# Performance work log

Hardware: AMD Instinct MI355X
Metric: run time of the kernel (lower is better)

The kernel has to match this reference:

```python
import jax, jax.numpy as jnp
import numpy as np

B, N, C, F = 64, 64, 8, 256      # batch, neighbors per sample, in_channels, in_features
OC, OF = 8, 256                  # out_channels, out_features


def setup_inputs() -> dict:
    key = jax.random.key(0)
    k0, k1, k2, k3, k4 = jax.random.split(key, 5)
    x = jax.random.normal(k0, (B, C, F), dtype=jnp.float32)
    neighbor = jax.random.normal(k1, (B, N, C, F), dtype=jnp.float32)
    # att1/att2: nn.Linear(in_features, in_channels, bias=False) -> weight (C, F)
    W1 = jax.random.normal(k2, (C, F), dtype=jnp.float32) * (1.0 / np.sqrt(F))
    W2 = jax.random.normal(k3, (C, F), dtype=jnp.float32) * (1.0 / np.sqrt(F))
    # conv: nn.Conv1d(C, OC*OF, kernel_size=F, bias=False) -> weight (OC*OF, C, F)
    Wc = jax.random.normal(k4, (OC * OF, C, F), dtype=jnp.float32) * (1.0 / np.sqrt(C * F))
    return {"x": x, "neighbor": neighbor, "W1": W1, "W2": W2, "Wc": Wc}


def _sgnroot(a):
    return jnp.sign(a) * jnp.sqrt(jnp.clip(jnp.abs(a), 1e-8))


def _row_normalize(a):
    # torch: x / (x.abs().sum(1, keepdim=True) + 1e-7); dim 1 is the channel dim of (B,C,F,F)
    a = a / (jnp.abs(a).sum(axis=1, keepdims=True) + 1e-7)
    return jnp.where(jnp.isnan(a), 0.0, a)


def _feature_adjacency(x, neighbor, W1, W2):
    # w[b,n] = sum_{c,k} (x[b] @ W1^T)[c,k] * sum_{k,l} (neighbor[b,n] @ W2^T)[k,l]
    s1 = jnp.einsum('bcf,kf->b', x, W1)            # total sum of att1(x[b])
    s2 = jnp.einsum('bncf,kf->bn', neighbor, W2)   # total sum of att2(y[b,n])
    w = s1[:, None] * s2                            # (B, N)
    # fadj[b,c,a,d] = sum_n x[b,c,a] * neighbor[b,n,c,d] * w[b,n]
    fadj = jnp.einsum('bca,bncd,bn->bcad', x, neighbor, w)
    fadj = fadj + jnp.swapaxes(fadj, -2, -1)
    return _row_normalize(_sgnroot(fadj))


def _conv_transform(z, Wc, lead_shape):
    # Conv1d(C, OC*OF, kernel_size=F, bias=False) over (.., C, F) == full contraction
    out = jnp.einsum('...cf,ocf->...o', z, Wc)
    return out.reshape(*lead_shape, OC, OF)


def reference(x, neighbor, W1, W2, Wc):
    adj = _feature_adjacency(x, neighbor, W1, W2)              # (B,C,F,F)
    # transform(x, adj): (adj @ x.unsqueeze(-1)).squeeze(-1) then conv
    zx = jnp.einsum('bcad,bcd->bca', adj, x)                   # (B,C,F)
    x_out = _conv_transform(zx, Wc, (x.shape[0],))             # (B,OC,OF)
    # transform(neighbor[i], adj[i:i+1]) for each i -> adj broadcasts over N
    zn = jnp.einsum('bcad,bncd->bnca', adj, neighbor)          # (B,N,C,F)
    n_out = _conv_transform(zn, Wc, (x.shape[0], neighbor.shape[1]))  # (B,N,OC,OF)
    return x_out, n_out
```

## Files before the change

### kernel.cpp

```cpp
#include <hip/hip_runtime.h>
#include <hip/hip_bf16.h>
#include <math.h>

#define B_ 64
#define N_ 64
#define C_ 8
#define F_ 256
#define K_ 2048
#define NO_ 2048
#define M_TOT 4160

typedef __attribute__((ext_vector_type(8))) short bf16x8;
typedef __attribute__((ext_vector_type(4))) float f32x4;

__global__ __launch_bounds__(256) void sums_wc_k(const float* __restrict__ x,
        const float* __restrict__ nb, const float* __restrict__ W1,
        const float* __restrict__ W2, const float* __restrict__ Wc,
        float* __restrict__ s1, float* __restrict__ s2,
        __hip_bfloat16* __restrict__ Bbuf) {
    int blk = blockIdx.x;
    int f = threadIdx.x;
    if (blk >= B_ * N_ + B_) {
        int i = (blk - (B_ * N_ + B_)) * 1024 + f * 4;
        float4 v = *(const float4*)(Wc + i);
        Bbuf[i + 0] = __float2bfloat16(v.x);
        Bbuf[i + 1] = __float2bfloat16(v.y);
        Bbuf[i + 2] = __float2bfloat16(v.z);
        Bbuf[i + 3] = __float2bfloat16(v.w);
        return;
    }
    float val;
    if (blk < B_ * N_) {
        const float* base = nb + (size_t)blk * (C_ * F_);
        float wsum = 0.f;
        #pragma unroll
        for (int k = 0; k < C_; ++k) wsum += W2[k * F_ + f];
        float cs = 0.f;
        #pragma unroll
        for (int c = 0; c < C_; ++c) cs += base[c * F_ + f];
        val = cs * wsum;
    } else {
        int b = blk - B_ * N_;
        const float* base = x + (size_t)b * (C_ * F_);
        float wsum = 0.f;
        #pragma unroll
        for (int k = 0; k < C_; ++k) wsum += W1[k * F_ + f];
        float cs = 0.f;
        #pragma unroll
        for (int c = 0; c < C_; ++c) cs += base[c * F_ + f];
        val = cs * wsum;
    }
    #pragma unroll
    for (int off = 32; off > 0; off >>= 1) val += __shfl_down(val, off, 64);
    __shared__ float wred[4];
    int w = f >> 6;
    if ((f & 63) == 0) wred[w] = val;
    __syncthreads();
    if (f == 0) {
        float s = wred[0] + wred[1] + wred[2] + wred[3];
        if (blk < B_ * N_) s2[blk] = s;
        else s1[blk - B_ * N_] = s;
    }
}

__global__ __launch_bounds__(1024) void t_k(const float* __restrict__ nb,
        const float* __restrict__ s1, const float* __restrict__ s2,
        float* __restrict__ t) {
    int blk = blockIdx.x;
    int b = blk / C_, c = blk % C_;
    int tid = threadIdx.x;
    int q = tid >> 8, d = tid & 255;
    const float* p = nb + ((size_t)(b * N_) * C_ + c) * F_ + d;
    const float* s2p = s2 + b * N_;
    float acc = 0.f;
    #pragma unroll
    for (int j = 0; j < 16; ++j) {
        int n = q * 16 + j;
        acc += p[(size_t)n * C_ * F_] * s2p[n];
    }
    __shared__ float part[4][F_];
    part[q][d] = acc;
    __syncthreads();
    if (tid < 256) {
        float s = part[0][d] + part[1][d] + part[2][d] + part[3][d];
        t[(size_t)blk * F_ + d] = s * s1[b];
    }
}

__global__ __launch_bounds__(256) void denom_k(const float* __restrict__ x,
        const float* __restrict__ t, float* __restrict__ rdenom) {
    int blk = blockIdx.x;
    int b = blk >> 8, a = blk & 255;
    int d = threadIdx.x;
    float acc = 1e-7f;
    #pragma unroll
    for (int c = 0; c < C_; ++c) {
        size_t o = ((size_t)b * C_ + c) * F_;
        float xa = x[o + a], ta = t[o + a];
        float xd = x[o + d], td = t[o + d];
        float v = xa * td + xd * ta;
        float r = __builtin_amdgcn_sqrtf(fmaxf(fabsf(v), 1e-8f));
        acc += (v != 0.f) ? r : 0.f;
    }
    rdenom[(size_t)blk * F_ + d] = __builtin_amdgcn_rcpf(acc);
}

__device__ __forceinline__ float sgnroot_dev(float v) {
    float r = __builtin_amdgcn_sqrtf(fmaxf(fabsf(v), 1e-8f));
    return (v > 0.f) ? r : ((v < 0.f) ? -r : 0.f);
}

#define ZNX_PAD 264
__global__ __launch_bounds__(256) void znx_k(const float* __restrict__ x,
        const float* __restrict__ t, const float* __restrict__ rdenom,
        const float* __restrict__ nb, __hip_bfloat16* __restrict__ Abuf) {
    int bc = blockIdx.x;
    int b = bc >> 3, c = bc & 7;
    int tid = threadIdx.x;
    int wave = tid >> 6, lane = tid & 63;
    __shared__ float xs[F_], ts[F_];
    __shared__ __hip_bfloat16 nbB[80 * ZNX_PAD];

    xs[tid] = x[(size_t)bc * F_ + tid];
    ts[tid] = t[(size_t)bc * F_ + tid];
    {
        int r = tid >> 2, cs0 = (tid & 3) * 64;
        const float* src = nb + (((size_t)(b * N_ + r)) * C_ + c) * F_ + cs0;
        __hip_bfloat16* dst = nbB + r * ZNX_PAD + cs0;
        #pragma unroll
        for (int j = 0; j < 64; j += 4) {
            float4 v = *(const float4*)(src + j);
            dst[j + 0] = __float2bfloat16(v.x);
            dst[j + 1] = __float2bfloat16(v.y);
            dst[j + 2] = __float2bfloat16(v.z);
            dst[j + 3] = __float2bfloat16(v.w);
        }
    }
    if (tid < 64) {
        float4 v = *(const float4*)(x + (size_t)bc * F_ + tid * 4);
        __hip_bfloat16* dst = nbB + 64 * ZNX_PAD + tid * 4;
        dst[0] = __float2bfloat16(v.x);
        dst[1] = __float2bfloat16(v.y);
        dst[2] = __float2bfloat16(v.z);
        dst[3] = __float2bfloat16(v.w);
    }
    {
        __hip_bfloat16 z = __float2bfloat16(0.f);
        #pragma unroll
        for (int j = 0; j < 16; ++j) {
            int o = 65 * ZNX_PAD + tid * 16 + j;
            if (o < 80 * ZNX_PAD) nbB[o] = z;
        }
    }
    __syncthreads();

    const int aq = lane & 15;
    const int dq = lane >> 4;
    #pragma unroll
    for (int atile = 0; atile < 4; ++atile) {
        int a = wave * 64 + atile * 16 + aq;
        float xa = xs[a], ta = ts[a];
        const float* drow = rdenom + ((size_t)b * F_ + a) * F_;
        f32x4 acc[5] = {};
        #pragma unroll
        for (int kc = 0; kc < 8; ++kc) {
            int d0 = kc * 32 + dq * 8;
            float4 xv0 = *(const float4*)(xs + d0);
            float4 xv1 = *(const float4*)(xs + d0 + 4);
            float4 tv0 = *(const float4*)(ts + d0);
            float4 tv1 = *(const float4*)(ts + d0 + 4);
            float4 dn0 = *(const float4*)(drow + d0);
            float4 dn1 = *(const float4*)(drow + d0 + 4);
            float xv[8] = {xv0.x, xv0.y, xv0.z, xv0.w, xv1.x, xv1.y, xv1.z, xv1.w};
            float tv[8] = {tv0.x, tv0.y, tv0.z, tv0.w, tv1.x, tv1.y, tv1.z, tv1.w};
            float dn[8] = {dn0.x, dn0.y, dn0.z, dn0.w, dn1.x, dn1.y, dn1.z, dn1.w};
            union { bf16x8 v; __hip_bfloat16 h[8]; } bu;
            #pragma unroll
            for (int j = 0; j < 8; ++j) {
                float g = sgnroot_dev(xa * tv[j] + xv[j] * ta);
                bu.h[j] = __float2bfloat16(g * dn[j]);
            }
            #pragma unroll
            for (int mt = 0; mt < 5; ++mt) {
                bf16x8 af = *(const bf16x8*)(nbB + (mt * 16 + aq) * ZNX_PAD
                                             + kc * 32 + dq * 8);
                acc[mt] = __builtin_amdgcn_mfma_f32_16x16x32_bf16(
                    af, bu.v, acc[mt], 0, 0, 0);
            }
        }
        int colA = c * F_ + a;
        #pragma unroll
        for (int mt = 0; mt < 4; ++mt) {
            int row = 64 + b * N_ + mt * 16 + dq * 4;
            #pragma unroll
            for (int i = 0; i < 4; ++i)
                Abuf[(size_t)(row + i) * K_ + colA] = __float2bfloat16(acc[mt][i]);
        }
        if (dq == 0)
            Abuf[(size_t)b * K_ + colA] = __float2bfloat16(acc[4][0]);
    }
}

__global__ __launch_bounds__(256) void gemm_bf16_k(
        const __hip_bfloat16* __restrict__ A,
        const __hip_bfloat16* __restrict__ Bm,
        float* __restrict__ Cm) {
    __shared__ char ldsA[8192] __attribute__((aligned(16)));
    __shared__ char ldsB[8192] __attribute__((aligned(16)));
    const int t = threadIdx.x;
    const int wave = t >> 6;
    const int lane = t & 63;
    const int col0 = blockIdx.x * 128;
    const int row0 = blockIdx.y * 128;
    const int wrow0 = (wave & 1) * 64;
    const int wcol0 = (wave >> 1) * 64;
    const int aq = lane & 15;
    const int dq = lane >> 4;

    const int rA0 = t >> 2;
    const int kcs = ((t & 3) - ((t >> 3) & 3)) & 3;
    const int kc = kcs * 8;
    const int grA0 = min(row0 + rA0, M_TOT - 1);
    const int grA1 = min(row0 + rA0 + 64, M_TOT - 1);
    const int gcB0 = col0 + rA0;
    const int gcB1 = col0 + rA0 + 64;
    char* lA0 = ldsA + wave * 1024;
    char* lA1 = ldsA + 4096 + wave * 1024;
    char* lB0 = ldsB + wave * 1024;
    char* lB1 = ldsB + 4096 + wave * 1024;

    const int swz = ((dq + (aq >> 1)) & 3) * 16;

    f32x4 acc[4][4] = {};

    for (int k0 = 0; k0 < K_; k0 += 32) {
        __syncthreads();
        __builtin_amdgcn_global_load_lds(
            (const __attribute__((address_space(1))) void*)(A + (size_t)grA0 * K_ + k0 + kc),
            (__attribute__((address_space(3))) void*)lA0, 16, 0, 0);
        __builtin_amdgcn_global_load_lds(
            (const __attribute__((address_space(1))) void*)(A + (size_t)grA1 * K_ + k0 + kc),
            (__attribute__((address_space(3))) void*)lA1, 16, 0, 0);
        __builtin_amdgcn_global_load_lds(
            (const __attribute__((address_space(1))) void*)(Bm + (size_t)gcB0 * K_ + k0 + kc),
            (__attribute__((address_space(3))) void*)lB0, 16, 0, 0);
        __builtin_amdgcn_global_load_lds(
            (const __attribute__((address_space(1))) void*)(Bm + (size_t)gcB1 * K_ + k0 + kc),
            (__attribute__((address_space(3))) void*)lB1, 16, 0, 0);
        __syncthreads();

        bf16x8 af[4], bf[4];
        #pragma unroll
        for (int rb = 0; rb < 4; ++rb)
            af[rb] = *(const bf16x8*)(ldsA + (wrow0 + rb * 16 + aq) * 64 + swz);
        #pragma unroll
        for (int cb = 0; cb < 4; ++cb)
            bf[cb] = *(const bf16x8*)(ldsB + (wcol0 + cb * 16 + aq) * 64 + swz);
        #pragma unroll
        for (int rb = 0; rb < 4; ++rb)
            #pragma unroll
            for (int cb = 0; cb < 4; ++cb)
                acc[rb][cb] = __builtin_amdgcn_mfma_f32_16x16x32_bf16(
                    af[rb], bf[cb], acc[rb][cb], 0, 0, 0);
    }

    #pragma unroll
    for (int rb = 0; rb < 4; ++rb) {
        int rowbase = row0 + wrow0 + rb * 16 + (lane >> 4) * 4;
        #pragma unroll
        for (int cb = 0; cb < 4; ++cb) {
            int col = col0 + wcol0 + cb * 16 + (lane & 15);
            #pragma unroll
            for (int i = 0; i < 4; ++i) {
                int row = rowbase + i;
                if (row < M_TOT)
                    Cm[(size_t)row * NO_ + col] = acc[rb][cb][i];
            }
        }
    }
}

extern "C" void kernel_launch(void* const* d_in, const int* in_sizes, int n_in,
                              void* d_out, int out_size, void* d_ws, size_t ws_size,
                              hipStream_t stream) {
    const float* x  = (const float*)d_in[0];
    const float* nb = (const float*)d_in[1];
    const float* W1 = (const float*)d_in[2];
    const float* W2 = (const float*)d_in[3];
    const float* Wc = (const float*)d_in[4];
    float* out = (float*)d_out;
    float* ws = (float*)d_ws;

    float* s1    = ws;
    float* s2    = ws + 64;
    float* t     = ws + 4160;
    float* rden  = ws + 135232;
    __hip_bfloat16* Abuf = (__hip_bfloat16*)(ws + 4329536);
    __hip_bfloat16* Bbuf = Abuf + (size_t)M_TOT * K_;

    hipLaunchKernelGGL(sums_wc_k, dim3(B_ * N_ + B_ + (K_ * NO_) / 1024),
                       dim3(256), 0, stream, x, nb, W1, W2, Wc, s1, s2, Bbuf);
    hipLaunchKernelGGL(t_k, dim3(B_ * C_), dim3(1024), 0, stream, nb, s1, s2, t);
    hipLaunchKernelGGL(denom_k, dim3(B_ * F_), dim3(256), 0, stream, x, t, rden);
    hipLaunchKernelGGL(znx_k, dim3(B_ * C_), dim3(256), 0, stream,
                       x, t, rden, nb, Abuf);
    hipLaunchKernelGGL(gemm_bf16_k, dim3(16, 33), dim3(256), 0, stream,
                       Abuf, Bbuf, out);
}
```

Before: 234.7 us.

## Triple-buffer GEMM LDS tiles with async global-to-LDS prefetch pipeline

Replaces the single-buffered LDS tiles of the bf16 MFMA GEMM with a three-stage ring buffer, issuing global_load_lds for up to two tiles ahead while computing the current one. Explicit vmcnt waits and barriers replace the two __syncthreads per K step, so memory latency can overlap with MFMA work. LDS use grows to 48KB per block, which may reduce occupancy, and the hand-counted vmcnt values must match the four loads issued per stage.

```diff
diff --git a/kernel.cpp b/kernel.cpp
--- a/kernel.cpp
+++ b/kernel.cpp
@@ -205,8 +205,7 @@
         const __hip_bfloat16* __restrict__ A,
         const __hip_bfloat16* __restrict__ Bm,
         float* __restrict__ Cm) {
-    __shared__ char ldsA[8192] __attribute__((aligned(16)));
-    __shared__ char ldsB[8192] __attribute__((aligned(16)));
+    __shared__ char lds[49152] __attribute__((aligned(16)));
     const int t = threadIdx.x;
     const int wave = t >> 6;
     const int lane = t & 63;
@@ -224,45 +223,92 @@
     const int grA1 = min(row0 + rA0 + 64, M_TOT - 1);
     const int gcB0 = col0 + rA0;
     const int gcB1 = col0 + rA0 + 64;
-    char* lA0 = ldsA + wave * 1024;
-    char* lA1 = ldsA + 4096 + wave * 1024;
-    char* lB0 = ldsB + wave * 1024;
-    char* lB1 = ldsB + 4096 + wave * 1024;
-
+    const size_t aoff0 = (size_t)grA0 * K_ + kc;
+    const size_t aoff1 = (size_t)grA1 * K_ + kc;
+    const size_t boff0 = (size_t)gcB0 * K_ + kc;
+    const size_t boff1 = (size_t)gcB1 * K_ + kc;
     const int swz = ((dq + (aq >> 1)) & 3) * 16;
+    const int ldsw = wave * 1024;
 
     f32x4 acc[4][4] = {};
 
-    for (int k0 = 0; k0 < K_; k0 += 32) {
-        __syncthreads();
-        __builtin_amdgcn_global_load_lds(
-            (const __attribute__((address_space(1))) void*)(A + (size_t)grA0 * K_ + k0 + kc),
-            (__attribute__((address_space(3))) void*)lA0, 16, 0, 0);
-        __builtin_amdgcn_global_load_lds(
-            (const __attribute__((address_space(1))) void*)(A + (size_t)grA1 * K_ + k0 + kc),
-            (__attribute__((address_space(3))) void*)lA1, 16, 0, 0);
-        __builtin_amdgcn_global_load_lds(
-            (const __attribute__((address_space(1))) void*)(Bm + (size_t)gcB0 * K_ + k0 + kc),
-            (__attribute__((address_space(3))) void*)lB0, 16, 0, 0);
-        __builtin_amdgcn_global_load_lds(
-            (const __attribute__((address_space(1))) void*)(Bm + (size_t)gcB1 * K_ + k0 + kc),
-            (__attribute__((address_space(3))) void*)lB1, 16, 0, 0);
-        __syncthreads();
-
-        bf16x8 af[4], bf[4];
-        #pragma unroll
-        for (int rb = 0; rb < 4; ++rb)
-            af[rb] = *(const bf16x8*)(ldsA + (wrow0 + rb * 16 + aq) * 64 + swz);
-        #pragma unroll
-        for (int cb = 0; cb < 4; ++cb)
-            bf[cb] = *(const bf16x8*)(ldsB + (wcol0 + cb * 16 + aq) * 64 + swz);
-        #pragma unroll
-        for (int rb = 0; rb < 4; ++rb)
-            #pragma unroll
-            for (int cb = 0; cb < 4; ++cb)
-                acc[rb][cb] = __builtin_amdgcn_mfma_f32_16x16x32_bf16(
-                    af[rb], bf[cb], acc[rb][cb], 0, 0, 0);
-    }
+#define STAGE(BI, TK) do {                                                     \
+    const int k0_ = (TK) * 32;                                                 \
+    char* la_ = lds + (BI) * 16384 + ldsw;                                     \
+    char* lb_ = la_ + 8192;                                                    \
+    __builtin_amdgcn_global_load_lds(                                          \
+        (const __attribute__((address_space(1))) void*)(A + aoff0 + k0_),      \
+        (__attribute__((address_space(3))) void*)la_, 16, 0, 0);               \
+    __builtin_amdgcn_global_load_lds(                                          \
+        (const __attribute__((address_space(1))) void*)(A + aoff1 + k0_),      \
+        (__attribute__((address_space(3))) void*)(la_ + 4096), 16, 0, 0);      \
+    __builtin_amdgcn_global_load_lds(                                          \
+        (const __attribute__((address_space(1))) void*)(Bm + boff0 + k0_),     \
+        (__attribute__((address_space(3))) void*)lb_, 16, 0, 0);               \
+    __builtin_amdgcn_global_load_lds(                                          \
+        (const __attribute__((address_space(1))) void*)(Bm + boff1 + k0_),     \
+        (__attribute__((address_space(3))) void*)(lb_ + 4096), 16, 0, 0);      \
+} while (0)
+
+#define COMPUTE(BI) do {                                                       \
+    const char* la_ = lds + (BI) * 16384;                                      \
+    const char* lb_ = la_ + 8192;                                              \
+    bf16x8 af_[4], bf_[4];                                                     \
+    _Pragma("unroll")                                                          \
+    for (int rb = 0; rb < 4; ++rb)                                             \
+        af_[rb] = *(const bf16x8*)(la_ + (wrow0 + rb * 16 + aq) * 64 + swz);   \
+    _Pragma("unroll")                                                          \
+    for (int cb = 0; cb < 4; ++cb)                                             \
+        bf_[cb] = *(const bf16x8*)(lb_ + (wcol0 + cb * 16 + aq) * 64 + swz);   \
+    _Pragma("unroll")                                                          \
+    for (int rb = 0; rb < 4; ++rb)                                             \
+        _Pragma("unroll")                                                      \
+        for (int cb = 0; cb < 4; ++cb)                                         \
+            acc[rb][cb] = __builtin_amdgcn_mfma_f32_16x16x32_bf16(             \
+                af_[rb], bf_[cb], acc[rb][cb], 0, 0, 0);                       \
+} while (0)
+
+#define WAIT_PIPE(N) do {                                                      \
+    asm volatile("s_waitcnt vmcnt(" #N ")" ::: "memory");                      \
+    __builtin_amdgcn_sched_barrier(0);                                         \
+    __builtin_amdgcn_s_barrier();                                              \
+    __builtin_amdgcn_sched_barrier(0);                                         \
+} while (0)
+
+    STAGE(0, 0);
+    STAGE(1, 1);
+    STAGE(2, 2);
+
+    for (int t3 = 0; t3 < 60; t3 += 3) {
+        WAIT_PIPE(8);
+        COMPUTE(0);
+        __builtin_amdgcn_s_barrier();
+        STAGE(0, t3 + 3);
+
+        WAIT_PIPE(8);
+        COMPUTE(1);
+        __builtin_amdgcn_s_barrier();
+        STAGE(1, t3 + 4);
+
+        WAIT_PIPE(8);
+        COMPUTE(2);
+        __builtin_amdgcn_s_barrier();
+        STAGE(2, t3 + 5);
+    }
+    WAIT_PIPE(8);
+    COMPUTE(0);
+    __builtin_amdgcn_s_barrier();
+    STAGE(0, 63);
+    WAIT_PIPE(8);
+    COMPUTE(1);
+    WAIT_PIPE(4);
+    COMPUTE(2);
+    WAIT_PIPE(0);
+    COMPUTE(0);
+
+#undef STAGE
+#undef COMPUTE
+#undef WAIT_PIPE
 
     #pragma unroll
     for (int rb = 0; rb < 4; ++rb) {
```

New measurement: 207.7 us. 1.13x faster.
